# Kernel optimization log

Measured on AMD Instinct MI355X. Metric: run time of the kernel, lower is better.

## Reference

```python
import jax, jax.numpy as jnp
import numpy as np

NUM_STREAMS = 4
DIM = 256
SINKHORN_ITERS = 10
SINKHORN_TAU = 0.05


def sinkhorn_log(logits, num_iters=SINKHORN_ITERS, tau=SINKHORN_TAU):
    n = logits.shape[-1]
    z = logits / tau
    log_marginal = -jnp.log(jnp.asarray(float(n), dtype=logits.dtype))

    def body(carry, _):
        u, v = carry
        u = log_marginal - jax.scipy.special.logsumexp(z + v[None, :], axis=1)
        v = log_marginal - jax.scipy.special.logsumexp(z + u[:, None], axis=0)
        return (u, v), None

    u0 = jnp.zeros((n,), dtype=z.dtype)
    v0 = jnp.zeros((n,), dtype=z.dtype)
    (u, v), _ = jax.lax.scan(body, (u0, v0), None, length=num_iters)
    return jnp.exp(z + u[:, None] + v[None, :]) * n


def setup_inputs() -> dict:
    key = jax.random.key(0)
    k_res, k_w = jax.random.split(key)
    B = 65536
    residuals = jax.random.normal(k_res, (B, NUM_STREAMS, DIM), dtype=jnp.float32)
    # h_res_logits: -8 everywhere, 0 on diagonal (as in __init__)
    h_res_logits = jnp.full((NUM_STREAMS, NUM_STREAMS), -8.0, dtype=jnp.float32)
    h_res_logits = h_res_logits.at[jnp.arange(NUM_STREAMS), jnp.arange(NUM_STREAMS)].set(0.0)
    # h_pre_logits: -8 everywhere, 0 at init_residual_index=0
    h_pre_logits = jnp.full((NUM_STREAMS,), -8.0, dtype=jnp.float32).at[0].set(0.0)
    h_post_logits = jnp.zeros((NUM_STREAMS,), dtype=jnp.float32)
    # branch Linear(dim, dim, bias=False): weight (out, in), y = x @ W.T
    bound = 1.0 / np.sqrt(DIM)
    W_branch = jax.random.uniform(k_w, (DIM, DIM), dtype=jnp.float32, minval=-bound, maxval=bound)
    return {
        "residuals": residuals,
        "h_res_logits": h_res_logits,
        "h_pre_logits": h_pre_logits,
        "h_post_logits": h_post_logits,
        "W_branch": W_branch,
    }


def reference(residuals, h_res_logits, h_pre_logits, h_post_logits, W_branch):
    # residuals: (B, S, D)
    h_res = sinkhorn_log(h_res_logits)                     # (S, S) doubly-stochastic * n
    h_pre = jax.nn.softmax(h_pre_logits)                   # (S,)
    h_post = jax.nn.softmax(h_post_logits)                 # (S,)
    residuals_mixed = jnp.einsum('st,bsd->btd', h_res, residuals)
    branch_input = jnp.einsum('s,bsd->bd', h_pre, residuals)
    branch_output = branch_input @ W_branch.T              # (B, D)
    depth_out = jnp.einsum('bd,s->bsd', branch_output, h_post)
    return residuals_mixed + depth_out
```

## Files before the change

kernel.cpp:

```cpp
#include <hip/hip_runtime.h>

#define NSTREAMS 4
#define DIM 256
#define BM 16
#define NTHREADS 1024
#define TILES 16

typedef __attribute__((ext_vector_type(8))) short short8;
typedef __attribute__((ext_vector_type(4))) float f32x4;

static __device__ __forceinline__ short f2bf(float x) {
    union { float f; unsigned int u; } c; c.f = x;
    unsigned int u = c.u;
    unsigned int lsb = (u >> 16) & 1u;
    u += 0x7fffu + lsb;
    return (short)(u >> 16);
}
static __device__ __forceinline__ int2 f2bf4(float4 v) {
    unsigned int lo, hi;
    asm("v_cvt_pk_bf16_f32 %0, %1, %2" : "=v"(lo) : "v"(v.x), "v"(v.y));
    asm("v_cvt_pk_bf16_f32 %0, %1, %2" : "=v"(hi) : "v"(v.z), "v"(v.w));
    int2 r; r.x = (int)lo; r.y = (int)hi;
    return r;
}

static __device__ __forceinline__ float rfl(float x) {
    int i = __builtin_amdgcn_readfirstlane(__builtin_bit_cast(int, x));
    return __builtin_bit_cast(float, i);
}

static __device__ __forceinline__ void barrier_lgkm() {
    asm volatile("s_waitcnt lgkmcnt(0)\n\ts_barrier" ::: "memory");
}

static __device__ void compute_h(const float* __restrict__ hres_l,
                                 const float* __restrict__ hpre_l,
                                 const float* __restrict__ hpost_l,
                                 float* h_out) {
    const float inv_tau = 1.0f / 0.05f;
    float z[4][4];
    for (int i = 0; i < 4; ++i)
        for (int j = 0; j < 4; ++j)
            z[i][j] = hres_l[i * 4 + j] * inv_tau;
    float u[4] = {0.f, 0.f, 0.f, 0.f};
    float v[4] = {0.f, 0.f, 0.f, 0.f};
    const float logm = -logf(4.0f);
    for (int it = 0; it < 10; ++it) {
        for (int i = 0; i < 4; ++i) {
            float m = -1e30f;
            for (int j = 0; j < 4; ++j) m = fmaxf(m, z[i][j] + v[j]);
            float ss = 0.f;
            for (int j = 0; j < 4; ++j) ss += expf(z[i][j] + v[j] - m);
            u[i] = logm - (m + logf(ss));
        }
        for (int j = 0; j < 4; ++j) {
            float m = -1e30f;
            for (int i = 0; i < 4; ++i) m = fmaxf(m, z[i][j] + u[i]);
            float ss = 0.f;
            for (int i = 0; i < 4; ++i) ss += expf(z[i][j] + u[i] - m);
            v[j] = logm - (m + logf(ss));
        }
    }
    for (int i = 0; i < 4; ++i)
        for (int j = 0; j < 4; ++j)
            h_out[i * 4 + j] = expf(z[i][j] + u[i] + v[j]) * 4.0f;
    {
        float m = fmaxf(fmaxf(hpre_l[0], hpre_l[1]), fmaxf(hpre_l[2], hpre_l[3]));
        float e0 = expf(hpre_l[0] - m), e1 = expf(hpre_l[1] - m);
        float e2 = expf(hpre_l[2] - m), e3 = expf(hpre_l[3] - m);
        float ss = e0 + e1 + e2 + e3;
        h_out[16] = e0 / ss; h_out[17] = e1 / ss; h_out[18] = e2 / ss; h_out[19] = e3 / ss;
    }
    {
        float m = fmaxf(fmaxf(hpost_l[0], hpost_l[1]), fmaxf(hpost_l[2], hpost_l[3]));
        float e0 = expf(hpost_l[0] - m), e1 = expf(hpost_l[1] - m);
        float e2 = expf(hpost_l[2] - m), e3 = expf(hpost_l[3] - m);
        float ss = e0 + e1 + e2 + e3;
        h_out[20] = e0 / ss; h_out[21] = e1 / ss; h_out[22] = e2 / ss; h_out[23] = e3 / ss;
    }
}

__global__ void prep_h_kernel(const float* __restrict__ hres_l,
                              const float* __restrict__ hpre_l,
                              const float* __restrict__ hpost_l,
                              float* __restrict__ ws) {
    if (threadIdx.x == 0) compute_h(hres_l, hpre_l, hpost_l, ws);
}

__global__ __launch_bounds__(256) void prep_wh_kernel(const float* __restrict__ Wb,
                                                      short* __restrict__ wbf,
                                                      const float* __restrict__ hres_l,
                                                      const float* __restrict__ hpre_l,
                                                      const float* __restrict__ hpost_l,
                                                      float* __restrict__ ws_h) {
    int idx = blockIdx.x * 256 + threadIdx.x;
    float4 v = reinterpret_cast<const float4*>(Wb)[idx];
    reinterpret_cast<int2*>(wbf)[idx] = f2bf4(v);
    if (blockIdx.x == 0 && threadIdx.x == 0)
        compute_h(hres_l, hpre_l, hpost_l, ws_h);
}

template <bool USE_WSW>
__global__ __launch_bounds__(NTHREADS, 1) void fused_kernel(
    const float* __restrict__ res,
    const float* __restrict__ Wb,
    const short* __restrict__ wbf,
    const float* __restrict__ hptr,
    const float* __restrict__ hres_l,
    const float* __restrict__ hpre_l,
    const float* __restrict__ hpost_l,
    float* __restrict__ out)
{
    __shared__ __align__(16) short W_lds[DIM * DIM];
    __shared__ __align__(16) short bi_lds[BM][DIM + 8];
    __shared__ __align__(16) float bo_lds[BM][DIM + 4];
    __shared__ float h_sh[24];

    const int t  = threadIdx.x;
    const int d4 = t & 63;
    const int r0 = t >> 6;
    const int w  = t >> 6;
    const int l  = t & 63;
    const int lr = l & 15;
    const int lk = l >> 4;

    const long tile0 = (long)blockIdx.x * TILES;
    float4 cur[4];
    {
        const float4* p = reinterpret_cast<const float4*>(
            res + (tile0 * BM + r0) * (NSTREAMS * DIM)) + d4;
        cur[0] = p[0];
        cur[1] = p[64];
        cur[2] = p[128];
        cur[3] = p[192];
    }

    #pragma unroll
    for (int i = 0; i < 8; ++i) {
        int c = t * 8 + i;
        int row = c >> 5;
        int koff = (c & 31) * 16;
        int dst = (row << 9) | (koff ^ ((row & 7) << 4));
        int4 wv;
        if (USE_WSW) {
            wv = reinterpret_cast<const int4*>(wbf)[c];
        } else {
            const float4* wp = reinterpret_cast<const float4*>(Wb) + c * 2;
            float4 wa = wp[0], wb2 = wp[1];
            int2 loq = f2bf4(wa), hiq = f2bf4(wb2);
            wv.x = loq.x; wv.y = loq.y; wv.z = hiq.x; wv.w = hiq.y;
        }
        *reinterpret_cast<int4*>(reinterpret_cast<char*>(W_lds) + dst) = wv;
    }

    if (hptr) {
        if (t < 24) h_sh[t] = hptr[t];
    } else if (t == 0) {
        compute_h(hres_l, hpre_l, hpost_l, h_sh);
    }
    barrier_lgkm();

    const float hp0 = rfl(h_sh[16]), hp1 = rfl(h_sh[17]);
    const float hp2 = rfl(h_sh[18]), hp3 = rfl(h_sh[19]);
    float hres[4][4];
    #pragma unroll
    for (int s = 0; s < 4; ++s)
        #pragma unroll
        for (int tt = 0; tt < 4; ++tt)
            hres[s][tt] = rfl(h_sh[s * 4 + tt]);
    float hq[4] = {rfl(h_sh[20]), rfl(h_sh[21]), rfl(h_sh[22]), rfl(h_sh[23])};

    {
        float4 bi;
        bi.x = hp0 * cur[0].x + hp1 * cur[1].x + hp2 * cur[2].x + hp3 * cur[3].x;
        bi.y = hp0 * cur[0].y + hp1 * cur[1].y + hp2 * cur[2].y + hp3 * cur[3].y;
        bi.z = hp0 * cur[0].z + hp1 * cur[1].z + hp2 * cur[2].z + hp3 * cur[3].z;
        bi.w = hp0 * cur[0].w + hp1 * cur[1].w + hp2 * cur[2].w + hp3 * cur[3].w;
        *reinterpret_cast<int2*>(&bi_lds[r0][d4 * 4]) = f2bf4(bi);
    }
    barrier_lgkm();

    const int dcol = w * 16 + lr;
    const char* wbase = reinterpret_cast<const char*>(W_lds) + (dcol << 9);
    const int dswz = (dcol & 7) << 4;

    for (int ti = 0; ti < TILES; ++ti) {
        const bool more = (ti + 1 < TILES);

        float4 nx[4];
        if (more) {
            const float4* p = reinterpret_cast<const float4*>(
                res + ((tile0 + ti + 1) * BM + r0) * (NSTREAMS * DIM)) + d4;
            nx[0] = p[0];
            nx[1] = p[64];
            nx[2] = p[128];
            nx[3] = p[192];
        }
        __builtin_amdgcn_sched_barrier(0);

        f32x4 acc = {0.f, 0.f, 0.f, 0.f};
        #pragma unroll
        for (int k0 = 0; k0 < DIM; k0 += 32) {
            short8 a = *reinterpret_cast<const short8*>(&bi_lds[lr][k0 + lk * 8]);
            short8 b = *reinterpret_cast<const short8*>(
                wbase + ((k0 * 2 + lk * 16) ^ dswz));
            acc = __builtin_amdgcn_mfma_f32_16x16x32_bf16(a, b, acc, 0, 0, 0);
        }

        #pragma unroll
        for (int j = 0; j < 4; ++j)
            bo_lds[lk * 4 + j][dcol] = acc[j];

        barrier_lgkm();

        {
            float4 bo = *reinterpret_cast<const float4*>(&bo_lds[r0][d4 * 4]);
            float* obase = out + (((tile0 + ti) * BM + r0) * 4) * DIM + d4 * 4;
            #pragma unroll
            for (int tt = 0; tt < 4; ++tt) {
                float4 o;
                o.x = hq[tt] * bo.x + hres[0][tt] * cur[0].x + hres[1][tt] * cur[1].x
                    + hres[2][tt] * cur[2].x + hres[3][tt] * cur[3].x;
                o.y = hq[tt] * bo.y + hres[0][tt] * cur[0].y + hres[1][tt] * cur[1].y
                    + hres[2][tt] * cur[2].y + hres[3][tt] * cur[3].y;
                o.z = hq[tt] * bo.z + hres[0][tt] * cur[0].z + hres[1][tt] * cur[1].z
                    + hres[2][tt] * cur[2].z + hres[3][tt] * cur[3].z;
                o.w = hq[tt] * bo.w + hres[0][tt] * cur[0].w + hres[1][tt] * cur[1].w
                    + hres[2][tt] * cur[2].w + hres[3][tt] * cur[3].w;
                *reinterpret_cast<float4*>(obase + tt * DIM) = o;
            }
        }

        if (more) {
            float4 bi;
            bi.x = hp0 * nx[0].x + hp1 * nx[1].x + hp2 * nx[2].x + hp3 * nx[3].x;
            bi.y = hp0 * nx[0].y + hp1 * nx[1].y + hp2 * nx[2].y + hp3 * nx[3].y;
            bi.z = hp0 * nx[0].z + hp1 * nx[1].z + hp2 * nx[2].z + hp3 * nx[3].z;
            bi.w = hp0 * nx[0].w + hp1 * nx[1].w + hp2 * nx[2].w + hp3 * nx[3].w;
            *reinterpret_cast<int2*>(&bi_lds[r0][d4 * 4]) = f2bf4(bi);
            #pragma unroll
            for (int s = 0; s < 4; ++s)
                cur[s] = nx[s];
        }
        barrier_lgkm();
    }
}

extern "C" void kernel_launch(void* const* d_in, const int* in_sizes, int n_in,
                              void* d_out, int out_size, void* d_ws, size_t ws_size,
                              hipStream_t stream) {
    const float* res     = (const float*)d_in[0];
    const float* hres_l  = (const float*)d_in[1];
    const float* hpre_l  = (const float*)d_in[2];
    const float* hpost_l = (const float*)d_in[3];
    const float* Wb      = (const float*)d_in[4];
    float* out = (float*)d_out;

    const int Btot = in_sizes[0] / (NSTREAMS * DIM);
    const int grid = Btot / (BM * TILES);

    const size_t W_OFF = 256;
    const size_t need_h = 24 * sizeof(float);
    const size_t need_w = W_OFF + (size_t)DIM * DIM * sizeof(short);
    const bool has_h = ws_size >= need_h;
    const bool has_w = ws_size >= need_w;

    float* ws_h = (float*)d_ws;
    short* ws_w = (short*)((char*)d_ws + W_OFF);

    if (has_w) {
        prep_wh_kernel<<<(DIM * DIM / 4) / 256, 256, 0, stream>>>(
            Wb, ws_w, hres_l, hpre_l, hpost_l, ws_h);
        fused_kernel<true><<<grid, NTHREADS, 0, stream>>>(
            res, Wb, ws_w, ws_h, hres_l, hpre_l, hpost_l, out);
    } else if (has_h) {
        prep_h_kernel<<<1, 64, 0, stream>>>(hres_l, hpre_l, hpost_l, ws_h);
        fused_kernel<false><<<grid, NTHREADS, 0, stream>>>(
            res, Wb, nullptr, ws_h, hres_l, hpre_l, hpost_l, out);
    } else {
        fused_kernel<false><<<grid, NTHREADS, 0, stream>>>(
            res, Wb, nullptr, nullptr, hres_l, hpre_l, hpost_l, out);
    }
}
```

Before: 128.7 us.

## Deepen residual prefetch to two tiles ahead and precompute mixing partials

The tile loop is unrolled by two and uses two register buffers (A and B), so residual loads are issued two tiles ahead instead of one. This gives global loads more time to land behind the MFMA and barrier work. The h_res mixing partial sums are now computed while staging the branch input, so the epilogue only adds the scaled branch output before storing. The cost is higher register pressure from the second buffer and the stored partials, which could lower occupancy or cause spills.

```diff
diff --git a/kernel.cpp b/kernel.cpp
--- a/kernel.cpp
+++ b/kernel.cpp
@@ -125,14 +125,12 @@
     const int lk = l >> 4;
 
     const long tile0 = (long)blockIdx.x * TILES;
-    float4 cur[4];
-    {
-        const float4* p = reinterpret_cast<const float4*>(
-            res + (tile0 * BM + r0) * (NSTREAMS * DIM)) + d4;
-        cur[0] = p[0];
-        cur[1] = p[64];
-        cur[2] = p[128];
-        cur[3] = p[192];
+    const long rowbase = (tile0 * BM + r0) * (NSTREAMS * DIM);
+
+    float4 A0, A1, A2, A3;
+    {
+        const float4* p = reinterpret_cast<const float4*>(res + rowbase) + d4;
+        A0 = p[0]; A1 = p[64]; A2 = p[128]; A3 = p[192];
     }
 
     #pragma unroll
@@ -170,79 +168,135 @@
             hres[s][tt] = rfl(h_sh[s * 4 + tt]);
     float hq[4] = {rfl(h_sh[20]), rfl(h_sh[21]), rfl(h_sh[22]), rfl(h_sh[23])};
 
+    float4 B0, B1, B2, B3;
+    {
+        const float4* p = reinterpret_cast<const float4*>(
+            res + rowbase + 1 * BM * (NSTREAMS * DIM)) + d4;
+        B0 = p[0]; B1 = p[64]; B2 = p[128]; B3 = p[192];
+    }
+
+    float4 opart[4];
     {
         float4 bi;
-        bi.x = hp0 * cur[0].x + hp1 * cur[1].x + hp2 * cur[2].x + hp3 * cur[3].x;
-        bi.y = hp0 * cur[0].y + hp1 * cur[1].y + hp2 * cur[2].y + hp3 * cur[3].y;
-        bi.z = hp0 * cur[0].z + hp1 * cur[1].z + hp2 * cur[2].z + hp3 * cur[3].z;
-        bi.w = hp0 * cur[0].w + hp1 * cur[1].w + hp2 * cur[2].w + hp3 * cur[3].w;
+        bi.x = hp0 * A0.x + hp1 * A1.x + hp2 * A2.x + hp3 * A3.x;
+        bi.y = hp0 * A0.y + hp1 * A1.y + hp2 * A2.y + hp3 * A3.y;
+        bi.z = hp0 * A0.z + hp1 * A1.z + hp2 * A2.z + hp3 * A3.z;
+        bi.w = hp0 * A0.w + hp1 * A1.w + hp2 * A2.w + hp3 * A3.w;
         *reinterpret_cast<int2*>(&bi_lds[r0][d4 * 4]) = f2bf4(bi);
+        #pragma unroll
+        for (int tt = 0; tt < 4; ++tt) {
+            opart[tt].x = hres[0][tt] * A0.x + hres[1][tt] * A1.x + hres[2][tt] * A2.x + hres[3][tt] * A3.x;
+            opart[tt].y = hres[0][tt] * A0.y + hres[1][tt] * A1.y + hres[2][tt] * A2.y + hres[3][tt] * A3.y;
+            opart[tt].z = hres[0][tt] * A0.z + hres[1][tt] * A1.z + hres[2][tt] * A2.z + hres[3][tt] * A3.z;
+            opart[tt].w = hres[0][tt] * A0.w + hres[1][tt] * A1.w + hres[2][tt] * A2.w + hres[3][tt] * A3.w;
+        }
     }
     barrier_lgkm();
 
     const int dcol = w * 16 + lr;
     const char* wbase = reinterpret_cast<const char*>(W_lds) + (dcol << 9);
     const int dswz = (dcol & 7) << 4;
-
-    for (int ti = 0; ti < TILES; ++ti) {
-        const bool more = (ti + 1 < TILES);
-
-        float4 nx[4];
-        if (more) {
-            const float4* p = reinterpret_cast<const float4*>(
-                res + ((tile0 + ti + 1) * BM + r0) * (NSTREAMS * DIM)) + d4;
-            nx[0] = p[0];
-            nx[1] = p[64];
-            nx[2] = p[128];
-            nx[3] = p[192];
-        }
-        __builtin_amdgcn_sched_barrier(0);
-
-        f32x4 acc = {0.f, 0.f, 0.f, 0.f};
-        #pragma unroll
-        for (int k0 = 0; k0 < DIM; k0 += 32) {
-            short8 a = *reinterpret_cast<const short8*>(&bi_lds[lr][k0 + lk * 8]);
-            short8 b = *reinterpret_cast<const short8*>(
-                wbase + ((k0 * 2 + lk * 16) ^ dswz));
-            acc = __builtin_amdgcn_mfma_f32_16x16x32_bf16(a, b, acc, 0, 0, 0);
-        }
-
-        #pragma unroll
-        for (int j = 0; j < 4; ++j)
-            bo_lds[lk * 4 + j][dcol] = acc[j];
-
-        barrier_lgkm();
-
+    const long tstride = (long)BM * (NSTREAMS * DIM);
+
+    for (int ti = 0; ti < TILES; ti += 2) {
         {
-            float4 bo = *reinterpret_cast<const float4*>(&bo_lds[r0][d4 * 4]);
-            float* obase = out + (((tile0 + ti) * BM + r0) * 4) * DIM + d4 * 4;
+            if (ti + 2 < TILES) {
+                const float4* p = reinterpret_cast<const float4*>(
+                    res + rowbase + (ti + 2) * tstride) + d4;
+                A0 = p[0]; A1 = p[64]; A2 = p[128]; A3 = p[192];
+            }
+            __builtin_amdgcn_sched_barrier(0);
+            f32x4 acc = {0.f, 0.f, 0.f, 0.f};
             #pragma unroll
-            for (int tt = 0; tt < 4; ++tt) {
-                float4 o;
-                o.x = hq[tt] * bo.x + hres[0][tt] * cur[0].x + hres[1][tt] * cur[1].x
-                    + hres[2][tt] * cur[2].x + hres[3][tt] * cur[3].x;
-                o.y = hq[tt] * bo.y + hres[0][tt] * cur[0].y + hres[1][tt] * cur[1].y
-                    + hres[2][tt] * cur[2].y + hres[3][tt] * cur[3].y;
-                o.z = hq[tt] * bo.z + hres[0][tt] * cur[0].z + hres[1][tt] * cur[1].z
-                    + hres[2][tt] * cur[2].z + hres[3][tt] * cur[3].z;
-                o.w = hq[tt] * bo.w + hres[0][tt] * cur[0].w + hres[1][tt] * cur[1].w
-                    + hres[2][tt] * cur[2].w + hres[3][tt] * cur[3].w;
-                *reinterpret_cast<float4*>(obase + tt * DIM) = o;
-            }
-        }
-
-        if (more) {
-            float4 bi;
-            bi.x = hp0 * nx[0].x + hp1 * nx[1].x + hp2 * nx[2].x + hp3 * nx[3].x;
-            bi.y = hp0 * nx[0].y + hp1 * nx[1].y + hp2 * nx[2].y + hp3 * nx[3].y;
-            bi.z = hp0 * nx[0].z + hp1 * nx[1].z + hp2 * nx[2].z + hp3 * nx[3].z;
-            bi.w = hp0 * nx[0].w + hp1 * nx[1].w + hp2 * nx[2].w + hp3 * nx[3].w;
-            *reinterpret_cast<int2*>(&bi_lds[r0][d4 * 4]) = f2bf4(bi);
+            for (int k0 = 0; k0 < DIM; k0 += 32) {
+                short8 a = *reinterpret_cast<const short8*>(&bi_lds[lr][k0 + lk * 8]);
+                short8 b = *reinterpret_cast<const short8*>(
+                    wbase + ((k0 * 2 + lk * 16) ^ dswz));
+                acc = __builtin_amdgcn_mfma_f32_16x16x32_bf16(a, b, acc, 0, 0, 0);
+            }
             #pragma unroll
-            for (int s = 0; s < 4; ++s)
-                cur[s] = nx[s];
-        }
-        barrier_lgkm();
+            for (int j = 0; j < 4; ++j)
+                bo_lds[lk * 4 + j][dcol] = acc[j];
+            barrier_lgkm();
+            {
+                float4 bo = *reinterpret_cast<const float4*>(&bo_lds[r0][d4 * 4]);
+                float* obase = out + (((tile0 + ti) * BM + r0) * 4) * DIM + d4 * 4;
+                #pragma unroll
+                for (int tt = 0; tt < 4; ++tt) {
+                    float4 o;
+                    o.x = opart[tt].x + hq[tt] * bo.x;
+                    o.y = opart[tt].y + hq[tt] * bo.y;
+                    o.z = opart[tt].z + hq[tt] * bo.z;
+                    o.w = opart[tt].w + hq[tt] * bo.w;
+                    *reinterpret_cast<float4*>(obase + tt * DIM) = o;
+                }
+            }
+            {
+                float4 bi;
+                bi.x = hp0 * B0.x + hp1 * B1.x + hp2 * B2.x + hp3 * B3.x;
+                bi.y = hp0 * B0.y + hp1 * B1.y + hp2 * B2.y + hp3 * B3.y;
+                bi.z = hp0 * B0.z + hp1 * B1.z + hp2 * B2.z + hp3 * B3.z;
+                bi.w = hp0 * B0.w + hp1 * B1.w + hp2 * B2.w + hp3 * B3.w;
+                *reinterpret_cast<int2*>(&bi_lds[r0][d4 * 4]) = f2bf4(bi);
+                #pragma unroll
+                for (int tt = 0; tt < 4; ++tt) {
+                    opart[tt].x = hres[0][tt] * B0.x + hres[1][tt] * B1.x + hres[2][tt] * B2.x + hres[3][tt] * B3.x;
+                    opart[tt].y = hres[0][tt] * B0.y + hres[1][tt] * B1.y + hres[2][tt] * B2.y + hres[3][tt] * B3.y;
+                    opart[tt].z = hres[0][tt] * B0.z + hres[1][tt] * B1.z + hres[2][tt] * B2.z + hres[3][tt] * B3.z;
+                    opart[tt].w = hres[0][tt] * B0.w + hres[1][tt] * B1.w + hres[2][tt] * B2.w + hres[3][tt] * B3.w;
+                }
+            }
+            barrier_lgkm();
+        }
+        {
+            if (ti + 3 < TILES) {
+                const float4* p = reinterpret_cast<const float4*>(
+                    res + rowbase + (ti + 3) * tstride) + d4;
+                B0 = p[0]; B1 = p[64]; B2 = p[128]; B3 = p[192];
+            }
+            __builtin_amdgcn_sched_barrier(0);
+            f32x4 acc = {0.f, 0.f, 0.f, 0.f};
+            #pragma unroll
+            for (int k0 = 0; k0 < DIM; k0 += 32) {
+                short8 a = *reinterpret_cast<const short8*>(&bi_lds[lr][k0 + lk * 8]);
+                short8 b = *reinterpret_cast<const short8*>(
+                    wbase + ((k0 * 2 + lk * 16) ^ dswz));
+                acc = __builtin_amdgcn_mfma_f32_16x16x32_bf16(a, b, acc, 0, 0, 0);
+            }
+            #pragma unroll
+            for (int j = 0; j < 4; ++j)
+                bo_lds[lk * 4 + j][dcol] = acc[j];
+            barrier_lgkm();
+            {
+                float4 bo = *reinterpret_cast<const float4*>(&bo_lds[r0][d4 * 4]);
+                float* obase = out + (((tile0 + ti + 1) * BM + r0) * 4) * DIM + d4 * 4;
+                #pragma unroll
+                for (int tt = 0; tt < 4; ++tt) {
+                    float4 o;
+                    o.x = opart[tt].x + hq[tt] * bo.x;
+                    o.y = opart[tt].y + hq[tt] * bo.y;
+                    o.z = opart[tt].z + hq[tt] * bo.z;
+                    o.w = opart[tt].w + hq[tt] * bo.w;
+                    *reinterpret_cast<float4*>(obase + tt * DIM) = o;
+                }
+            }
+            if (ti + 2 < TILES) {
+                float4 bi;
+                bi.x = hp0 * A0.x + hp1 * A1.x + hp2 * A2.x + hp3 * A3.x;
+                bi.y = hp0 * A0.y + hp1 * A1.y + hp2 * A2.y + hp3 * A3.y;
+                bi.z = hp0 * A0.z + hp1 * A1.z + hp2 * A2.z + hp3 * A3.z;
+                bi.w = hp0 * A0.w + hp1 * A1.w + hp2 * A2.w + hp3 * A3.w;
+                *reinterpret_cast<int2*>(&bi_lds[r0][d4 * 4]) = f2bf4(bi);
+                #pragma unroll
+                for (int tt = 0; tt < 4; ++tt) {
+                    opart[tt].x = hres[0][tt] * A0.x + hres[1][tt] * A1.x + hres[2][tt] * A2.x + hres[3][tt] * A3.x;
+                    opart[tt].y = hres[0][tt] * A0.y + hres[1][tt] * A1.y + hres[2][tt] * A2.y + hres[3][tt] * A3.y;
+                    opart[tt].z = hres[0][tt] * A0.z + hres[1][tt] * A1.z + hres[2][tt] * A2.z + hres[3][tt] * A3.z;
+                    opart[tt].w = hres[0][tt] * A0.w + hres[1][tt] * A1.w + hres[2][tt] * A2.w + hres[3][tt] * A3.w;
+                }
+            }
+            barrier_lgkm();
+        }
     }
 }
 
```

Result: slower. 131.5 us (+2.1%).
